# Optimization experiments

Hardware: AMD Instinct MI355X
Metric: run time of the kernel (lower is better)

The kernel has to match this reference:

```python
import jax, jax.numpy as jnp
import numpy as np

# Module hyperparameters (from init_kwargs)
B, C, E, T = 8, 128, 128, 128          # batch, in_channels, embedding(freq), time
O, G, KW, KS = 256, 4, 9, 1            # out_channels, groups, kernel_width, kernel_stride
D = C // G                              # kernel depth per group = 32
N = O // G                              # filters per group = 64
AH, AS = 2, 2                           # activate_height, activate_stride
NEG_SLOPE = 0.01                        # nn.LeakyReLU default


def setup_inputs() -> dict:
    key = jax.random.key(0)
    kx, kw = jax.random.split(key)
    x = jax.random.normal(kx, (B, C, E, T), dtype=jnp.float32)
    # xavier_uniform over (O, D, E, KW): fan_in = D*E*KW, fan_out = O*E*KW
    fan_in, fan_out = D * E * KW, O * E * KW
    limit = float(np.sqrt(6.0 / (fan_in + fan_out)))
    weight = jax.random.uniform(kw, (O, D, E, KW), dtype=jnp.float32,
                                minval=-limit, maxval=limit)
    return {"x": x, "weight": weight}


def reference(x, weight):
    b, c, e, t = x.shape
    # --- symmetric-ish zero pad along time so unfold yields exactly t windows ---
    pad = (t - 1) * KS - t + KW
    xp = jnp.pad(x, ((0, 0), (0, 0), (0, 0), (pad // 2, (pad + 1) // 2)))
    # --- unfold: windows of size KW at stride KS -> (b, c, e, t, KW) ---
    idx = jnp.arange(t)[:, None] * KS + jnp.arange(KW)[None, :]  # (t, KW)
    xu = xp[..., idx]                                            # (b, c, e, t, KW)
    # --- grouped linear-conv: instead of materializing (b,t,g,n,d,e,KW), contract d,KW ---
    xu = xu.reshape(b, G, D, e, t, KW)                 # (b, g, d, e, t, w)
    wr = weight.reshape(G, N, D, e, KW)                # (g, n, d, e, w)
    # z[b,g,n,e,t] = sum_{d,w} xu * wr  (the all-ones conv sums over d and full width w)
    z = jnp.einsum('bgdetw,gndew->bgnet', xu, wr).reshape(b, O, e, t)
    # --- all-ones conv height pooling: kernel AH, stride AS over e (valid) ---
    f_out = (e - AH) // AS + 1
    cs = jnp.cumsum(z, axis=2)
    cs = jnp.concatenate([jnp.zeros_like(cs[:, :, :1]), cs], axis=2)  # prefix sums
    pos = jnp.arange(f_out) * AS
    pooled = cs[:, :, pos + AH, :] - cs[:, :, pos, :]   # (b, O, f_out, t)
    # --- LeakyReLU ---
    y = jnp.where(pooled >= 0, pooled, NEG_SLOPE * pooled)
    return y  # (b, o, f_out, t), matching 'b o f t'
```

## Files before the change

kernel.cpp:

```cpp
#include <hip/hip_runtime.h>
#include <cstddef>

typedef __attribute__((ext_vector_type(8))) short short8v;
typedef __attribute__((ext_vector_type(4))) short short4v;
typedef __attribute__((ext_vector_type(4))) float f32x4;

__device__ __forceinline__ unsigned short f2bf(float f) {
    unsigned u = __float_as_uint(f);
    u = (u + 0x7FFFu + ((u >> 16) & 1u)) >> 16;
    return (unsigned short)u;
}

__global__ __launch_bounds__(256) void prep_w(const float* __restrict__ w,
                                              unsigned short* __restrict__ wb)
{
    const int g  = blockIdx.x >> 6;
    const int f  = blockIdx.x & 63;
    const int e0 = 2 * f;
    const int tid = threadIdx.x;
    __shared__ unsigned short ls[64 * 580];

    #pragma unroll 4
    for (int i = 0; i < 72; ++i) {
        int fl  = tid + i * 256;
        int od  = fl / 9;
        int f2i = fl - od * 9;
        int o_l = od >> 5;
        int d   = od & 31;
        const float2 v = *reinterpret_cast<const float2*>(
            &w[(size_t)((g * 64 + o_l) * 32 + d) * 1152 + e0 * 9 + f2i * 2]);
        ushort2 hh; hh.x = f2bf(v.x); hh.y = f2bf(v.y);
        *reinterpret_cast<ushort2*>(&ls[o_l * 580 + d * 18 + f2i * 2]) = hh;
    }
    __syncthreads();

    unsigned short* wo = wb + (size_t)(g * 64 + f) * 36864;
    #pragma unroll 2
    for (int i = 0; i < 18; ++i) {
        int oc   = tid + i * 256;
        int ks   = oc >> 8;
        int nt   = (oc >> 6) & 3;
        int lane = oc & 63;
        int li = lane & 15, hi = lane >> 4;
        int e  = (ks >= 9) ? 1 : 0;
        int w9 = ks - 9 * e;
        int o_l = nt * 16 + li;
        short8v vv;
        #pragma unroll
        for (int j = 0; j < 8; ++j)
            vv[j] = (short)ls[o_l * 580 + (hi * 8 + j) * 18 + e * 9 + w9];
        *reinterpret_cast<short8v*>(&wo[(size_t)oc * 8]) = vv;
    }
}

__global__ __launch_bounds__(256, 1) void lconv_mfma(const float* __restrict__ x,
                                                     const unsigned short* __restrict__ wb,
                                                     float* __restrict__ out)
{
    extern __shared__ __align__(16) unsigned short smem[];
    unsigned short* As = smem;

    const int g  = blockIdx.x >> 6;
    const int f  = blockIdx.x & 63;
    const int e0 = 2 * f;

    const int tid  = threadIdx.x;
    const int lane = tid & 63;
    const int wv   = tid >> 6;
    const int li   = lane & 15;
    const int hi   = lane >> 4;

    unsigned short* xsw = smem + 36864 + wv * 10880;

    const unsigned short* wslab = wb + (size_t)(g * 64 + f) * 36864;
    #pragma unroll
    for (int i = 0; i < 18; ++i) {
        __builtin_amdgcn_global_load_lds(
            (const __attribute__((address_space(1))) void*)(wslab + i * 2048 + tid * 8),
            (__attribute__((address_space(3))) void*)(As + i * 2048 + tid * 8),
            16, 0, 0);
    }

    #pragma unroll
    for (int it = 0; it < 3; ++it) {
        int u = it * 64 + lane;
        if (u < 160) {
            int e  = u / 80;
            int r  = (u % 80) / 10;
            int dq = u % 10;
            int tp = (r < 4) ? r : (128 + r);
            short4v zz = {0, 0, 0, 0};
            *reinterpret_cast<short4v*>(&xsw[e * 5440 + tp * 40 + dq * 4]) = zz;
        }
    }

    float2 fr[32];
    auto issueX = [&](int b, int e) {
        const float* xp0 = &x[((size_t)(b * 128 + g * 32) * 128 + (e0 + e)) * 128 + 2 * lane];
        #pragma unroll
        for (int d = 0; d < 32; ++d)
            fr[d] = *reinterpret_cast<const float2*>(xp0 + (size_t)d * 16384);
    };
    auto lwriteX = [&](int e) {
        unsigned short* base = xsw + e * 5440 + (2 * lane + 4) * 40;
        #pragma unroll
        for (int dq = 0; dq < 8; ++dq) {
            short4v h0, h1;
            #pragma unroll
            for (int j = 0; j < 4; ++j) {
                h0[j] = (short)f2bf(fr[dq * 4 + j].x);
                h1[j] = (short)f2bf(fr[dq * 4 + j].y);
            }
            *reinterpret_cast<short4v*>(&base[dq * 4])      = h0;
            *reinterpret_cast<short4v*>(&base[40 + dq * 4]) = h1;
        }
    };

    const int b0 = wv, b1 = wv + 4;
    issueX(b0, 0); lwriteX(0);
    issueX(b0, 1); lwriteX(1);
    __syncthreads();

    f32x4 acc[4][8];
    #pragma unroll
    for (int nt = 0; nt < 4; ++nt)
        #pragma unroll
        for (int tt = 0; tt < 8; ++tt)
            acc[nt][tt] = (f32x4){0.f, 0.f, 0.f, 0.f};

    auto compute_half = [&](int e) {
        #pragma unroll
        for (int w9 = 0; w9 < 9; ++w9) {
            short8v Af[4], Bf[8];
            #pragma unroll
            for (int nt = 0; nt < 4; ++nt)
                Af[nt] = *reinterpret_cast<const short8v*>(
                    &As[(e * 9 + w9) * 2048 + nt * 512 + lane * 8]);
            #pragma unroll
            for (int tt = 0; tt < 8; ++tt) {
                int tp = tt * 16 + li + w9;
                Bf[tt] = *reinterpret_cast<const short8v*>(
                    &xsw[e * 5440 + tp * 40 + hi * 8]);
            }
            __builtin_amdgcn_s_setprio(1);
            #pragma unroll
            for (int nt = 0; nt < 4; ++nt)
                #pragma unroll
                for (int tt = 0; tt < 8; ++tt)
                    acc[nt][tt] = __builtin_amdgcn_mfma_f32_16x16x32_bf16(
                        Af[nt], Bf[tt], acc[nt][tt], 0, 0, 0);
            __builtin_amdgcn_s_setprio(0);
        }
    };

    auto store_b = [&](int b) {
        #pragma unroll
        for (int nt = 0; nt < 4; ++nt)
            #pragma unroll
            for (int tt = 0; tt < 8; ++tt)
                #pragma unroll
                for (int j = 0; j < 4; ++j) {
                    float v = acc[nt][tt][j];
                    v = (v >= 0.f) ? v : 0.01f * v;
                    int n  = nt * 16 + hi * 4 + j;
                    int tc = tt * 16 + li;
                    out[(((size_t)(b * 256 + g * 64 + n)) * 64 + f) * 128 + tc] = v;
                    acc[nt][tt][j] = 0.f;
                }
    };

    issueX(b1, 0);
    compute_half(0);
    lwriteX(0);
    issueX(b1, 1);
    compute_half(1);
    store_b(b0);
    lwriteX(1);

    compute_half(0);
    compute_half(1);
    store_b(b1);
}

extern "C" void kernel_launch(void* const* d_in, const int* in_sizes, int n_in,
                              void* d_out, int out_size, void* d_ws, size_t ws_size,
                              hipStream_t stream)
{
    const float* x = (const float*)d_in[0];
    const float* w = (const float*)d_in[1];
    float* out = (float*)d_out;
    unsigned short* wb = (unsigned short*)d_ws;

    (void)hipFuncSetAttribute((const void*)lconv_mfma,
                              hipFuncAttributeMaxDynamicSharedMemorySize, 160768);

    hipLaunchKernelGGL(prep_w, dim3(256), dim3(256), 0, stream, w, wb);
    hipLaunchKernelGGL(lconv_mfma, dim3(256), dim3(256), 160768, stream, x, wb, out);
}
```

Before: 53.31 us.

## Warp-specialize lconv kernel into producer and MFMA consumer waves

```diff
diff --git a/kernel.cpp b/kernel.cpp
--- a/kernel.cpp
+++ b/kernel.cpp
@@ -53,12 +53,13 @@
     }
 }
 
-__global__ __launch_bounds__(256, 1) void lconv_mfma(const float* __restrict__ x,
+__global__ __launch_bounds__(512, 1) void lconv_mfma(const float* __restrict__ x,
                                                      const unsigned short* __restrict__ wb,
                                                      float* __restrict__ out)
 {
     extern __shared__ __align__(16) unsigned short smem[];
     unsigned short* As = smem;
+    unsigned short* xs = smem + 36864;
 
     const int g  = blockIdx.x >> 6;
     const int f  = blockIdx.x & 63;
@@ -70,39 +71,42 @@
     const int li   = lane & 15;
     const int hi   = lane >> 4;
 
-    unsigned short* xsw = smem + 36864 + wv * 10880;
-
     const unsigned short* wslab = wb + (size_t)(g * 64 + f) * 36864;
     #pragma unroll
-    for (int i = 0; i < 18; ++i) {
+    for (int i = 0; i < 9; ++i) {
         __builtin_amdgcn_global_load_lds(
-            (const __attribute__((address_space(1))) void*)(wslab + i * 2048 + tid * 8),
-            (__attribute__((address_space(3))) void*)(As + i * 2048 + tid * 8),
+            (const __attribute__((address_space(1))) void*)(wslab + i * 4096 + tid * 8),
+            (__attribute__((address_space(3))) void*)(As + i * 4096 + tid * 8),
             16, 0, 0);
     }
 
     #pragma unroll
-    for (int it = 0; it < 3; ++it) {
-        int u = it * 64 + lane;
-        if (u < 160) {
-            int e  = u / 80;
-            int r  = (u % 80) / 10;
-            int dq = u % 10;
-            int tp = (r < 4) ? r : (128 + r);
+    for (int it = 0; it < 2; ++it) {
+        int u = it * 512 + tid;
+        if (u < 640) {
+            int slab = u / 160;
+            int rem  = u % 160;
+            int e    = rem / 80;
+            int r    = (rem % 80) / 10;
+            int dq   = rem % 10;
+            int tp   = (r < 4) ? r : (128 + r);
             short4v zz = {0, 0, 0, 0};
-            *reinterpret_cast<short4v*>(&xsw[e * 5440 + tp * 40 + dq * 4]) = zz;
-        }
-    }
-
+            *reinterpret_cast<short4v*>(
+                &xs[slab * 10880 + e * 5440 + tp * 40 + dq * 4]) = zz;
+        }
+    }
+
+    const int blz = wv & 1;
+    const int pe  = (wv >> 1) & 1;
     float2 fr[32];
-    auto issueX = [&](int b, int e) {
-        const float* xp0 = &x[((size_t)(b * 128 + g * 32) * 128 + (e0 + e)) * 128 + 2 * lane];
+
+    auto pstage = [&](int pair, int set) {
+        const int b = pair * 2 + blz;
+        const float* xp0 = &x[((size_t)(b * 128 + g * 32) * 128 + (e0 + pe)) * 128 + 2 * lane];
         #pragma unroll
         for (int d = 0; d < 32; ++d)
             fr[d] = *reinterpret_cast<const float2*>(xp0 + (size_t)d * 16384);
-    };
-    auto lwriteX = [&](int e) {
-        unsigned short* base = xsw + e * 5440 + (2 * lane + 4) * 40;
+        unsigned short* base = xs + set * 21760 + blz * 10880 + pe * 5440 + (2 * lane + 4) * 40;
         #pragma unroll
         for (int dq = 0; dq < 8; ++dq) {
             short4v h0, h1;
@@ -116,70 +120,69 @@
         }
     };
 
-    const int b0 = wv, b1 = wv + 4;
-    issueX(b0, 0); lwriteX(0);
-    issueX(b0, 1); lwriteX(1);
-    __syncthreads();
-
-    f32x4 acc[4][8];
+    const int bl = wv & 1;
+    const int th = wv >> 1;
+    f32x4 acc[4][4];
     #pragma unroll
     for (int nt = 0; nt < 4; ++nt)
         #pragma unroll
-        for (int tt = 0; tt < 8; ++tt)
+        for (int tt = 0; tt < 4; ++tt)
             acc[nt][tt] = (f32x4){0.f, 0.f, 0.f, 0.f};
 
-    auto compute_half = [&](int e) {
-        #pragma unroll
-        for (int w9 = 0; w9 < 9; ++w9) {
-            short8v Af[4], Bf[8];
+    auto compute_pair = [&](int pair, int set) {
+        const unsigned short* xb = xs + set * 21760 + bl * 10880;
+        #pragma unroll
+        for (int e = 0; e < 2; ++e) {
             #pragma unroll
-            for (int nt = 0; nt < 4; ++nt)
-                Af[nt] = *reinterpret_cast<const short8v*>(
-                    &As[(e * 9 + w9) * 2048 + nt * 512 + lane * 8]);
-            #pragma unroll
-            for (int tt = 0; tt < 8; ++tt) {
-                int tp = tt * 16 + li + w9;
-                Bf[tt] = *reinterpret_cast<const short8v*>(
-                    &xsw[e * 5440 + tp * 40 + hi * 8]);
+            for (int w9 = 0; w9 < 9; ++w9) {
+                short8v Af[4], Bf[4];
+                #pragma unroll
+                for (int nt = 0; nt < 4; ++nt)
+                    Af[nt] = *reinterpret_cast<const short8v*>(
+                        &As[(e * 9 + w9) * 2048 + nt * 512 + lane * 8]);
+                #pragma unroll
+                for (int tt = 0; tt < 4; ++tt) {
+                    int tp = th * 64 + tt * 16 + li + w9;
+                    Bf[tt] = *reinterpret_cast<const short8v*>(
+                        &xb[e * 5440 + tp * 40 + hi * 8]);
+                }
+                __builtin_amdgcn_s_setprio(1);
+                #pragma unroll
+                for (int nt = 0; nt < 4; ++nt)
+                    #pragma unroll
+                    for (int tt = 0; tt < 4; ++tt)
+                        acc[nt][tt] = __builtin_amdgcn_mfma_f32_16x16x32_bf16(
+                            Af[nt], Bf[tt], acc[nt][tt], 0, 0, 0);
+                __builtin_amdgcn_s_setprio(0);
             }
-            __builtin_amdgcn_s_setprio(1);
-            #pragma unroll
-            for (int nt = 0; nt < 4; ++nt)
-                #pragma unroll
-                for (int tt = 0; tt < 8; ++tt)
-                    acc[nt][tt] = __builtin_amdgcn_mfma_f32_16x16x32_bf16(
-                        Af[nt], Bf[tt], acc[nt][tt], 0, 0, 0);
-            __builtin_amdgcn_s_setprio(0);
-        }
-    };
-
-    auto store_b = [&](int b) {
+        }
+        const int b = pair * 2 + bl;
         #pragma unroll
         for (int nt = 0; nt < 4; ++nt)
             #pragma unroll
-            for (int tt = 0; tt < 8; ++tt)
+            for (int tt = 0; tt < 4; ++tt)
                 #pragma unroll
                 for (int j = 0; j < 4; ++j) {
                     float v = acc[nt][tt][j];
                     v = (v >= 0.f) ? v : 0.01f * v;
                     int n  = nt * 16 + hi * 4 + j;
-                    int tc = tt * 16 + li;
+                    int tc = th * 64 + tt * 16 + li;
                     out[(((size_t)(b * 256 + g * 64 + n)) * 64 + f) * 128 + tc] = v;
                     acc[nt][tt][j] = 0.f;
                 }
     };
 
-    issueX(b1, 0);
-    compute_half(0);
-    lwriteX(0);
-    issueX(b1, 1);
-    compute_half(1);
-    store_b(b0);
-    lwriteX(1);
-
-    compute_half(0);
-    compute_half(1);
-    store_b(b1);
+    if (wv >= 4) pstage(0, 0);
+    __syncthreads();
+
+    for (int p = 0; p < 4; ++p) {
+        if (wv < 4) {
+            compute_pair(p, p & 1);
+        } else if (p < 3) {
+            pstage(p + 1, (p + 1) & 1);
+        }
+        __syncthreads();
+    }
 }
 
 extern "C" void kernel_launch(void* const* d_in, const int* in_sizes, int n_in,
@@ -195,5 +198,5 @@
                               hipFuncAttributeMaxDynamicSharedMemorySize, 160768);
 
     hipLaunchKernelGGL(prep_w, dim3(256), dim3(256), 0, stream, w, wb);
-    hipLaunchKernelGGL(lconv_mfma, dim3(256), dim3(256), 160768, stream, x, wb, out);
-}
+    hipLaunchKernelGGL(lconv_mfma, dim3(256), dim3(512), 160768, stream, x, wb, out);
+}
```

Result: no change. 53.60 us (+0.6%).
